# Optimization experiments

Measured on AMD Instinct MI355X. Metric: run time of the kernel, lower is better.

Reference implementation:

```python
import jax, jax.numpy as jnp
import numpy as np

NEG_SLOPE = 0.2
N_NODES = 50000
N_EDGES = 800000
IN_DIM = 256
HID_DIM = 256
HEADS = 8
HEAD_DIM = HID_DIM // HEADS


def setup_inputs() -> dict:
    key = jax.random.key(0)
    ks = jax.random.split(key, 12)
    def glorot(k, shape):
        fan = sum(shape[-2:]) if len(shape) > 1 else shape[-1] + 1
        return jax.random.normal(k, shape, jnp.float32) * jnp.sqrt(2.0 / fan)
    return {
        "data": jax.random.normal(ks[0], (N_NODES, IN_DIM), jnp.float32),
        "src": jax.random.randint(ks[1], (N_EDGES,), 0, N_NODES),
        "dst": jax.random.randint(ks[2], (N_EDGES,), 0, N_NODES),
        "W1": glorot(ks[3], (IN_DIM, HID_DIM)),
        "al1": glorot(ks[4], (HEADS, HEAD_DIM)),
        "ar1": glorot(ks[5], (HEADS, HEAD_DIM)),
        "b1": jnp.zeros((HID_DIM,), jnp.float32),
        "W2": glorot(ks[6], (HID_DIM, HID_DIM)),
        "al2": glorot(ks[7], (HEADS, HEAD_DIM)),
        "ar2": glorot(ks[8], (HEADS, HEAD_DIM)),
        "b2": jnp.zeros((HID_DIM,), jnp.float32),
    }


def gat_layer(x, src, dst, W, al, ar, b):
    """One DGL-style GATConv layer with ReLU activation."""
    N = x.shape[0]
    feat = (x @ W).reshape(N, HEADS, HEAD_DIM)            # [N,H,D]
    el = jnp.sum(feat * al[None], axis=-1)                # [N,H]
    er = jnp.sum(feat * ar[None], axis=-1)                # [N,H]
    e = el[src] + er[dst]                                  # [E,H]
    e = jnp.where(e > 0, e, NEG_SLOPE * e)                 # LeakyReLU(0.2)
    # segment softmax over incoming edges of each dst node
    m = jax.ops.segment_max(e, dst, num_segments=N)        # [N,H] (-inf for empty)
    a = jnp.exp(e - m[dst])                                # [E,H]
    denom = jax.ops.segment_sum(a, dst, num_segments=N)    # [N,H]
    alpha = a / denom[dst]                                 # [E,H]
    msg = feat[src] * alpha[:, :, None]                    # [E,H,D]
    out = jax.ops.segment_sum(msg, dst, num_segments=N)    # [N,H,D]
    out = out + b.reshape(1, HEADS, HEAD_DIM)
    out = jax.nn.relu(out)
    return out.reshape(N, HID_DIM)


def reference(data, src, dst, W1, al1, ar1, b1, W2, al2, ar2, b2):
    h = gat_layer(data, src, dst, W1, al1, ar1, b1)
    h = gat_layer(h, src, dst, W2, al2, ar2, b2)
    return h
```

## Files before the change

kernel.cpp:

```cpp
#include <hip/hip_runtime.h>

#define N_NODES 50000
#define N_EDGES 800000
#define DIM 256
#define HEADS 8
#define NEG_SLOPE 0.2f

typedef unsigned short u16;
typedef float floatx4 __attribute__((ext_vector_type(4)));
typedef __bf16 bf16x8 __attribute__((ext_vector_type(8)));

__device__ __forceinline__ float b2f(u16 u) {
    union { unsigned int i; float f; } v; v.i = ((unsigned int)u) << 16; return v.f;
}
__device__ __forceinline__ u16 f2b(float f) {
    union { float f; unsigned int i; } v; v.f = f;
    unsigned int x = v.i;
    if ((x & 0x7f800000u) == 0x7f800000u && (x & 0x007fffffu)) {
        return (u16)((x >> 16) | 0x0040u);
    }
    unsigned int r = (x + 0x7fffu + ((x >> 16) & 1u)) >> 16;
    return (u16)r;
}

__global__ __launch_bounds__(256) void fill_u32(unsigned int* __restrict__ p,
                                                unsigned int v, int n) {
    int i = blockIdx.x * 256 + threadIdx.x;
    if (i < n) p[i] = v;
}

__global__ __launch_bounds__(256) void init_kernel(const unsigned int* __restrict__ d,
                                                   int* __restrict__ counts,
                                                   int* __restrict__ flag) {
    int i = blockIdx.x * 256 + threadIdx.x;
    if (i < N_NODES) counts[i] = 0;
    if (blockIdx.x == 0) {
        __shared__ int cnt;
        if (threadIdx.x == 0) cnt = 0;
        __syncthreads();
        unsigned int w = d[threadIdx.x];
        int bad = 0;
        #pragma unroll
        for (int half = 0; half < 2; ++half) {
            u16 u = (u16)(w >> (16 * half));
            unsigned int e = (u >> 7) & 0xFFu;
            if (u != 0 && (e >= 141u || e <= 27u)) bad = 1;
        }
        atomicAdd(&cnt, bad);
        __syncthreads();
        if (threadIdx.x == 0) *flag = (cnt > 64) ? 1 : 0;
    }
}

__global__ __launch_bounds__(256) void prep_kernel(const void* __restrict__ W1,
                                                   const void* __restrict__ W2,
                                                   const void* __restrict__ data,
                                                   u16* __restrict__ Wt1,
                                                   u16* __restrict__ Wt2,
                                                   u16* __restrict__ datab,
                                                   const int* __restrict__ flagp) {
    const int isf = *flagp;
    int b = blockIdx.x;
    if (b < 32) {
        const void* W = (b < 16) ? W1 : W2;
        u16* Wt = (b < 16) ? Wt1 : Wt2;
        int t = b & 15;
        int k0 = (t >> 2) * 64, n0 = (t & 3) * 64;
        __shared__ float lt[64][65];
        int c = threadIdx.x & 63, r0 = threadIdx.x >> 6;
        #pragma unroll
        for (int j = 0; j < 16; ++j) {
            int r = j * 4 + r0;
            lt[r][c] = isf ? ((const float*)W)[(k0 + r) * 256 + n0 + c]
                           : b2f(((const u16*)W)[(k0 + r) * 256 + n0 + c]);
        }
        __syncthreads();
        #pragma unroll
        for (int j = 0; j < 16; ++j) {
            int rn = j * 4 + r0;
            Wt[(n0 + rn) * 256 + k0 + c] = f2b(lt[c][rn]);
        }
    } else {
        if (!isf) return;
        int base = (b - 32) * 2048 + threadIdx.x * 8;
        const float* df = (const float*)data + base;
        float4 f0 = *(const float4*)df;
        float4 f1 = *(const float4*)(df + 4);
        u16 tb[8] = {f2b(f0.x), f2b(f0.y), f2b(f0.z), f2b(f0.w),
                     f2b(f1.x), f2b(f1.y), f2b(f1.z), f2b(f1.w)};
        *(uint4*)(datab + base) = *(uint4*)tb;
    }
}

__global__ __launch_bounds__(256) void hist_kernel(const int* __restrict__ dst,
                                                   int* __restrict__ counts, int E) {
    int i = blockIdx.x * 256 + threadIdx.x;
    if (i < E) atomicAdd(&counts[dst[i]], 1);
}

__global__ __launch_bounds__(256) void scan_partial(const int* __restrict__ counts,
                                                    int* __restrict__ partial, int n) {
    int b = blockIdx.x, tid = threadIdx.x;
    int base = b * 1024 + tid * 4;
    int s = 0;
    #pragma unroll
    for (int k = 0; k < 4; ++k) if (base + k < n) s += counts[base + k];
    int lane = tid & 63;
    #pragma unroll
    for (int off = 32; off; off >>= 1) s += __shfl_xor(s, off);
    __shared__ int wsum[4];
    if (lane == 0) wsum[tid >> 6] = s;
    __syncthreads();
    if (tid == 0) partial[b] = wsum[0] + wsum[1] + wsum[2] + wsum[3];
}

__global__ __launch_bounds__(64) void scan_offsets(const int* __restrict__ partial,
                                                   int* __restrict__ offsets,
                                                   int* __restrict__ row_ptr,
                                                   int nb, int n) {
    int t = threadIdx.x;
    int v0 = (t < nb) ? partial[t] : 0;
    int v = v0;
    #pragma unroll
    for (int d = 1; d < 64; d <<= 1) {
        int u = __shfl_up(v, d);
        if (t >= d) v += u;
    }
    if (t < nb) offsets[t] = v - v0;
    if (t == 63) row_ptr[n] = v;
}

__global__ __launch_bounds__(256) void scan_write(const int* __restrict__ counts,
                                                  const int* __restrict__ offsets,
                                                  int* __restrict__ row_ptr,
                                                  int* __restrict__ wptr, int n) {
    int b = blockIdx.x, tid = threadIdx.x;
    int base = b * 1024 + tid * 4;
    int v[4]; int s = 0;
    #pragma unroll
    for (int k = 0; k < 4; ++k) { v[k] = (base + k < n) ? counts[base + k] : 0; s += v[k]; }
    int lane = tid & 63, w = tid >> 6;
    int incl = s;
    #pragma unroll
    for (int d = 1; d < 64; d <<= 1) {
        int u = __shfl_up(incl, d);
        if (lane >= d) incl += u;
    }
    __shared__ int wsum[4];
    if (lane == 63) wsum[w] = incl;
    __syncthreads();
    int woff = 0;
    for (int i = 0; i < w; ++i) woff += wsum[i];
    int run = offsets[b] + woff + incl - s;
    #pragma unroll
    for (int k = 0; k < 4; ++k) {
        if (base + k < n) { row_ptr[base + k] = run; wptr[base + k] = run; run += v[k]; }
    }
}

__global__ __launch_bounds__(256) void scatter_kernel(const int* __restrict__ src,
                                                      const int* __restrict__ dst,
                                                      int* __restrict__ wptr,
                                                      int* __restrict__ src_sorted, int E) {
    int i = blockIdx.x * 256 + threadIdx.x;
    if (i < E) {
        int pos = atomicAdd(&wptr[dst[i]], 1);
        src_sorted[pos] = src[i];
    }
}

#define LDA 264
#define LDB 40

__global__ __launch_bounds__(256, 2) void gemm_fused(const u16* __restrict__ Aisf,
                                                     const u16* __restrict__ Abf,
                                                     const u16* __restrict__ Wt,
                                                     u16* __restrict__ outF,
                                                     float* __restrict__ el,
                                                     float* __restrict__ er,
                                                     const void* __restrict__ al,
                                                     const void* __restrict__ ar,
                                                     int M, const int* __restrict__ flagp) {
    const int isf = *flagp;
    const u16* A = isf ? Aisf : Abf;
    __shared__ u16 As[64][LDA];
    __shared__ u16 Ws[256][LDB];
    const int tid  = threadIdx.x;
    const int w    = tid >> 6;
    const int lane = tid & 63;
    const int quad = lane >> 4;
    const int l16  = lane & 15;
    const int m0   = blockIdx.x * 64;

    #pragma unroll
    for (int it = 0; it < 8; ++it) {
        int idx = it * 256 + tid;
        int r = idx >> 5;
        int c = (idx & 31) << 3;
        int gr = m0 + r;
        if (gr < M) {
            *(uint4*)&As[r][c] = *(const uint4*)(A + gr * 256 + c);
        } else {
            uint4 z = {0u, 0u, 0u, 0u};
            *(uint4*)&As[r][c] = z;
        }
    }

    floatx4 acc[4][4] = {};

    for (int s = 0; s < 8; ++s) {
        __syncthreads();
        #pragma unroll
        for (int it = 0; it < 4; ++it) {
            int idx = it * 256 + tid;
            int n = idx >> 2;
            int k8 = (idx & 3) << 3;
            *(uint4*)&Ws[n][k8] = *(const uint4*)(Wt + n * 256 + s * 32 + k8);
        }
        __syncthreads();

        bf16x8 af[4], bfv[4];
        #pragma unroll
        for (int i = 0; i < 4; ++i)
            af[i] = *(const bf16x8*)&As[16 * i + l16][s * 32 + quad * 8];
        #pragma unroll
        for (int t = 0; t < 4; ++t)
            bfv[t] = *(const bf16x8*)&Ws[64 * w + 16 * t + l16][quad * 8];
        #pragma unroll
        for (int i = 0; i < 4; ++i)
            #pragma unroll
            for (int t = 0; t < 4; ++t)
                acc[i][t] = __builtin_amdgcn_mfma_f32_16x16x32_bf16(af[i], bfv[t], acc[i][t], 0, 0, 0);
    }

    #pragma unroll
    for (int i = 0; i < 4; ++i)
        #pragma unroll
        for (int t = 0; t < 4; ++t)
            #pragma unroll
            for (int r = 0; r < 4; ++r) {
                int row = m0 + 16 * i + quad * 4 + r;
                if (row < M) outF[row * 256 + 64 * w + 16 * t + l16] = f2b(acc[i][t][r]);
            }

    float alv[4], arv[4];
    #pragma unroll
    for (int t = 0; t < 4; ++t) {
        int c = 64 * w + 16 * t + l16;
        alv[t] = isf ? ((const float*)al)[c] : b2f(((const u16*)al)[c]);
        arv[t] = isf ? ((const float*)ar)[c] : b2f(((const u16*)ar)[c]);
    }
    #pragma unroll
    for (int i = 0; i < 4; ++i)
        #pragma unroll
        for (int r = 0; r < 4; ++r) {
            int row = m0 + 16 * i + quad * 4 + r;
            #pragma unroll
            for (int tt = 0; tt < 2; ++tt) {
                float pl = acc[i][2 * tt][r] * alv[2 * tt] + acc[i][2 * tt + 1][r] * alv[2 * tt + 1];
                float pr = acc[i][2 * tt][r] * arv[2 * tt] + acc[i][2 * tt + 1][r] * arv[2 * tt + 1];
                #pragma unroll
                for (int mask = 1; mask <= 8; mask <<= 1) {
                    pl += __shfl_xor(pl, mask);
                    pr += __shfl_xor(pr, mask);
                }
                if (l16 == 0 && row < M) {
                    el[row * 8 + 2 * w + tt] = pl;
                    er[row * 8 + 2 * w + tt] = pr;
                }
            }
        }
}

__global__ __launch_bounds__(256) void aggregate_kernel(const u16* __restrict__ feat,
                                                        const float* __restrict__ el,
                                                        const float* __restrict__ er,
                                                        const void* __restrict__ bias,
                                                        const int* __restrict__ row_ptr,
                                                        const int* __restrict__ src_sorted,
                                                        void* __restrict__ out,
                                                        int out_mode,
                                                        const int* __restrict__ flagp) {
    const int isf = *flagp;
    const int lane = threadIdx.x & 63;
    const int node = blockIdx.x * 4 + (threadIdx.x >> 6);
    if (node >= N_NODES) return;
    const int h = lane >> 3;
    const int j = lane & 7;
    const int beg = row_ptr[node];
    const int deg = row_ptr[node + 1] - beg;
    const float ern = er[node * HEADS + h];

    float m = -1e30f, ssum = 0.f;
    for (int i = j; i < deg; i += 8) {
        int s = src_sorted[beg + i];
        float e = el[s * 8 + h] + ern;
        e = e > 0.f ? e : NEG_SLOPE * e;
        float mn = fmaxf(m, e);
        ssum = ssum * __expf(m - mn) + __expf(e - mn);
        m = mn;
    }
    #pragma unroll
    for (int mask = 1; mask <= 4; mask <<= 1) {
        float mo = __shfl_xor(m, mask);
        float so = __shfl_xor(ssum, mask);
        float mn = fmaxf(m, mo);
        ssum = ssum * __expf(m - mn) + so * __expf(mo - mn);
        m = mn;
    }
    const float mx = m;
    const float inv = ssum > 0.f ? 1.f / ssum : 0.f;

    const int q = lane & 31;
    const int half = lane >> 5;
    const int hq = q >> 2;
    float a[8] = {};
    for (int c0 = 0; c0 < deg; c0 += 8) {
        int i = c0 + j;
        int s = 0; float av = 0.f;
        if (i < deg) {
            s = src_sorted[beg + i];
            float e = el[s * 8 + h] + ern;
            e = e > 0.f ? e : NEG_SLOPE * e;
            av = __expf(e - mx) * inv;
        }
        int rem = deg - c0; if (rem > 8) rem = 8;
        for (int t2 = 0; t2 < rem; t2 += 2) {
            int sel = hq * 8 + t2 + half;
            int   se = __shfl(s, sel);
            float ae = __shfl(av, sel);
            uint4 f = *(const uint4*)(feat + se * DIM + 8 * q);
            a[0] += ae * b2f((u16)(f.x & 0xffffu)); a[1] += ae * b2f((u16)(f.x >> 16));
            a[2] += ae * b2f((u16)(f.y & 0xffffu)); a[3] += ae * b2f((u16)(f.y >> 16));
            a[4] += ae * b2f((u16)(f.z & 0xffffu)); a[5] += ae * b2f((u16)(f.z >> 16));
            a[6] += ae * b2f((u16)(f.w & 0xffffu)); a[7] += ae * b2f((u16)(f.w >> 16));
        }
    }
    #pragma unroll
    for (int k = 0; k < 8; ++k) a[k] += __shfl_xor(a[k], 32);

    if (half == 0) {
        float o[8];
        if (isf) {
            float4 b0 = *(const float4*)((const float*)bias + 8 * q);
            float4 b1 = *(const float4*)((const float*)bias + 8 * q + 4);
            o[0] = a[0] + b0.x; o[1] = a[1] + b0.y; o[2] = a[2] + b0.z; o[3] = a[3] + b0.w;
            o[4] = a[4] + b1.x; o[5] = a[5] + b1.y; o[6] = a[6] + b1.z; o[7] = a[7] + b1.w;
        } else {
            uint4 bu = *(const uint4*)((const u16*)bias + 8 * q);
            o[0] = a[0] + b2f((u16)(bu.x & 0xffffu)); o[1] = a[1] + b2f((u16)(bu.x >> 16));
            o[2] = a[2] + b2f((u16)(bu.y & 0xffffu)); o[3] = a[3] + b2f((u16)(bu.y >> 16));
            o[4] = a[4] + b2f((u16)(bu.z & 0xffffu)); o[5] = a[5] + b2f((u16)(bu.z >> 16));
            o[6] = a[6] + b2f((u16)(bu.w & 0xffffu)); o[7] = a[7] + b2f((u16)(bu.w >> 16));
        }
        #pragma unroll
        for (int k = 0; k < 8; ++k) o[k] = fmaxf(o[k], 0.f);
        if (out_mode == 0 || !isf) {
            u16 pk[8] = {f2b(o[0]), f2b(o[1]), f2b(o[2]), f2b(o[3]),
                         f2b(o[4]), f2b(o[5]), f2b(o[6]), f2b(o[7])};
            *(uint4*)((u16*)out + node * DIM + 8 * q) = *(uint4*)pk;
        } else {
            float4 v0 = {o[0], o[1], o[2], o[3]};
            float4 v1 = {o[4], o[5], o[6], o[7]};
            *(float4*)((float*)out + node * DIM + 8 * q) = v0;
            *(float4*)((float*)out + node * DIM + 8 * q + 4) = v1;
        }
    }
}

extern "C" void kernel_launch(void* const* d_in, const int* in_sizes, int n_in,
                              void* d_out, int out_size, void* d_ws, size_t ws_size,
                              hipStream_t stream) {
    const void* data = d_in[0];
    const int* src = (const int*)d_in[1];
    const int* dst = (const int*)d_in[2];
    const void* W1  = d_in[3];
    const void* al1 = d_in[4];
    const void* ar1 = d_in[5];
    const void* b1  = d_in[6];
    const void* W2  = d_in[7];
    const void* al2 = d_in[8];
    const void* ar2 = d_in[9];
    const void* b2  = d_in[10];

    const size_t NEEDED =
        (size_t)N_NODES * DIM * 2 +
        (size_t)N_NODES * HEADS * 4 * 2 +
        (size_t)N_NODES * 4 * 2 +
        (size_t)(N_NODES + 4) * 4 +
        (size_t)N_EDGES * 4 +
        2 * 256 * 256 * 2 +
        1024;

    if (ws_size < NEEDED) {
        int nwords = (out_size + 1) / 2;
        fill_u32<<<(nwords + 255) / 256, 256, 0, stream>>>(
            (unsigned int*)d_out, 0x42C842C8u, nwords);
        return;
    }

    char* ws = (char*)d_ws;
    u16* feat = (u16*)ws;        ws += (size_t)N_NODES * DIM * 2;
    float* el = (float*)ws;      ws += (size_t)N_NODES * HEADS * 4;
    float* er = (float*)ws;      ws += (size_t)N_NODES * HEADS * 4;
    int* counts = (int*)ws;      ws += (size_t)N_NODES * 4;
    int* wptr = (int*)ws;        ws += (size_t)N_NODES * 4;
    int* row_ptr = (int*)ws;     ws += (size_t)(N_NODES + 4) * 4;
    int* src_sorted = (int*)ws;  ws += (size_t)N_EDGES * 4;
    u16* Wt1 = (u16*)ws;         ws += 256 * 256 * 2;
    u16* Wt2 = (u16*)ws;         ws += 256 * 256 * 2;
    int* partial = (int*)ws;     ws += 256;
    int* offsets = (int*)ws;     ws += 256;
    int* flag = (int*)ws;        ws += 256;

    u16* h1    = (u16*)d_out;
    u16* datab = (u16*)d_out + (size_t)N_NODES * DIM;

    const int nb = (N_NODES + 1023) / 1024;

    init_kernel<<<(N_NODES + 255) / 256, 256, 0, stream>>>(
        (const unsigned int*)data, counts, flag);
    prep_kernel<<<32 + (N_NODES * DIM) / 2048, 256, 0, stream>>>(
        W1, W2, data, Wt1, Wt2, datab, flag);
    hist_kernel<<<(N_EDGES + 255) / 256, 256, 0, stream>>>(dst, counts, N_EDGES);
    scan_partial<<<nb, 256, 0, stream>>>(counts, partial, N_NODES);
    scan_offsets<<<1, 64, 0, stream>>>(partial, offsets, row_ptr, nb, N_NODES);
    scan_write<<<nb, 256, 0, stream>>>(counts, offsets, row_ptr, wptr, N_NODES);
    scatter_kernel<<<(N_EDGES + 255) / 256, 256, 0, stream>>>(src, dst, wptr, src_sorted, N_EDGES);

    const int gemm_blocks = (N_NODES + 63) / 64;
    const int agg_blocks = (N_NODES + 3) / 4;

    gemm_fused<<<gemm_blocks, 256, 0, stream>>>(datab, (const u16*)data, Wt1, feat,
                                                el, er, al1, ar1, N_NODES, flag);
    aggregate_kernel<<<agg_blocks, 256, 0, stream>>>(feat, el, er, b1, row_ptr, src_sorted,
                                                     (void*)h1, 0, flag);
    gemm_fused<<<gemm_blocks, 256, 0, stream>>>(h1, h1, Wt2, feat,
                                                el, er, al2, ar2, N_NODES, flag);
    aggregate_kernel<<<agg_blocks, 256, 0, stream>>>(feat, el, er, b2, row_ptr, src_sorted,
                                                     d_out, 2, flag);
}
```

Baseline: 437.2 us.

## Split aggregation across head-quarters and cache edge scores in shared memory

The aggregation kernel now launches four times as many blocks, and each wave handles one node for only two heads (a quarter of the feature columns), with 32 lanes per head in the softmax reduction. Source indices and edge logits for the first 96 edges are cached in LDS and turned into normalised attention weights once, so the weighted-sum loop reads them instead of recomputing from el. Each feature gather becomes a 16-byte slice per lane covering 8 edges at a time. The cost is four times the src_sorted/el reads per node across blocks, plus extra cross-lane reductions.

```diff
diff --git a/kernel.cpp b/kernel.cpp
--- a/kernel.cpp
+++ b/kernel.cpp
@@ -5,6 +5,7 @@
 #define DIM 256
 #define HEADS 8
 #define NEG_SLOPE 0.2f
+#define CAP 96
 
 typedef unsigned short u16;
 typedef float floatx4 __attribute__((ext_vector_type(4)));
@@ -282,72 +283,116 @@
                                                         int out_mode,
                                                         const int* __restrict__ flagp) {
     const int isf = *flagp;
+    const int NB4 = (N_NODES + 3) / 4;
+    const int qtr = blockIdx.x / NB4;
+    const int wv = threadIdx.x >> 6;
+    const int node = (blockIdx.x % NB4) * 4 + wv;
+    if (node >= N_NODES) return;
     const int lane = threadIdx.x & 63;
-    const int node = blockIdx.x * 4 + (threadIdx.x >> 6);
-    if (node >= N_NODES) return;
-    const int h = lane >> 3;
-    const int j = lane & 7;
+
+    __shared__ int   sS[4][CAP];
+    __shared__ float sE[4][CAP][2];
+
     const int beg = row_ptr[node];
     const int deg = row_ptr[node + 1] - beg;
-    const float ern = er[node * HEADS + h];
-
+
+    const int half = lane >> 5;
+    const int t = lane & 31;
+    const int h = 2 * qtr + half;
+    const float ern = er[node * 8 + h];
     float m = -1e30f, ssum = 0.f;
-    for (int i = j; i < deg; i += 8) {
+    for (int i = t; i < deg; i += 32) {
         int s = src_sorted[beg + i];
         float e = el[s * 8 + h] + ern;
         e = e > 0.f ? e : NEG_SLOPE * e;
+        if (i < CAP) {
+            if (half == 0) sS[wv][i] = s;
+            sE[wv][i][half] = e;
+        }
         float mn = fmaxf(m, e);
         ssum = ssum * __expf(m - mn) + __expf(e - mn);
         m = mn;
     }
     #pragma unroll
-    for (int mask = 1; mask <= 4; mask <<= 1) {
+    for (int mask = 1; mask <= 16; mask <<= 1) {
         float mo = __shfl_xor(m, mask);
         float so = __shfl_xor(ssum, mask);
         float mn = fmaxf(m, mo);
         ssum = ssum * __expf(m - mn) + so * __expf(mo - mn);
         m = mn;
     }
-    const float mx = m;
     const float inv = ssum > 0.f ? 1.f / ssum : 0.f;
 
-    const int q = lane & 31;
-    const int half = lane >> 5;
-    const int hq = q >> 2;
+    const int dcap = deg < CAP ? deg : CAP;
+    for (int i = t; i < dcap; i += 32) {
+        sE[wv][i][half] = __expf(sE[wv][i][half] - m) * inv;
+    }
+
+    const float mxA = __shfl(m, 0),  invA = __shfl(inv, 0),  ernA = __shfl(ern, 0);
+    const float mxB = __shfl(m, 32), invB = __shfl(inv, 32), ernB = __shfl(ern, 32);
+
+    const int j = lane & 7;
+    const int slot = lane >> 3;
+    const int hsel = j >> 2;
+    const float mxs  = hsel ? mxB : mxA;
+    const float invs = hsel ? invB : invA;
+    const float erns = hsel ? ernB : ernA;
+    const int hidx = 2 * qtr + hsel;
+    const u16* fbase = feat + qtr * 64 + j * 8;
+
     float a[8] = {};
-    for (int c0 = 0; c0 < deg; c0 += 8) {
-        int i = c0 + j;
-        int s = 0; float av = 0.f;
-        if (i < deg) {
-            s = src_sorted[beg + i];
-            float e = el[s * 8 + h] + ern;
-            e = e > 0.f ? e : NEG_SLOPE * e;
-            av = __expf(e - mx) * inv;
-        }
-        int rem = deg - c0; if (rem > 8) rem = 8;
-        for (int t2 = 0; t2 < rem; t2 += 2) {
-            int sel = hq * 8 + t2 + half;
-            int   se = __shfl(s, sel);
-            float ae = __shfl(av, sel);
-            uint4 f = *(const uint4*)(feat + se * DIM + 8 * q);
-            a[0] += ae * b2f((u16)(f.x & 0xffffu)); a[1] += ae * b2f((u16)(f.x >> 16));
-            a[2] += ae * b2f((u16)(f.y & 0xffffu)); a[3] += ae * b2f((u16)(f.y >> 16));
-            a[4] += ae * b2f((u16)(f.z & 0xffffu)); a[5] += ae * b2f((u16)(f.z >> 16));
-            a[6] += ae * b2f((u16)(f.w & 0xffffu)); a[7] += ae * b2f((u16)(f.w >> 16));
-        }
-    }
-    #pragma unroll
-    for (int k = 0; k < 8; ++k) a[k] += __shfl_xor(a[k], 32);
-
-    if (half == 0) {
+    for (int c0 = 0; c0 < deg; c0 += 16) {
+        int iA = c0 + slot;
+        int iB = c0 + 8 + slot;
+        int sA = 0, sB = 0;
+        float aeA = 0.f, aeB = 0.f;
+        if (iA < deg) {
+            if (iA < CAP) { sA = sS[wv][iA]; aeA = sE[wv][iA][hsel]; }
+            else {
+                sA = src_sorted[beg + iA];
+                float e = el[sA * 8 + hidx] + erns;
+                e = e > 0.f ? e : NEG_SLOPE * e;
+                aeA = __expf(e - mxs) * invs;
+            }
+        }
+        if (iB < deg) {
+            if (iB < CAP) { sB = sS[wv][iB]; aeB = sE[wv][iB][hsel]; }
+            else {
+                sB = src_sorted[beg + iB];
+                float e = el[sB * 8 + hidx] + erns;
+                e = e > 0.f ? e : NEG_SLOPE * e;
+                aeB = __expf(e - mxs) * invs;
+            }
+        }
+        uint4 fA = *(const uint4*)(fbase + (size_t)sA * DIM);
+        uint4 fB = *(const uint4*)(fbase + (size_t)sB * DIM);
+        a[0] += aeA * b2f((u16)(fA.x & 0xffffu)); a[1] += aeA * b2f((u16)(fA.x >> 16));
+        a[2] += aeA * b2f((u16)(fA.y & 0xffffu)); a[3] += aeA * b2f((u16)(fA.y >> 16));
+        a[4] += aeA * b2f((u16)(fA.z & 0xffffu)); a[5] += aeA * b2f((u16)(fA.z >> 16));
+        a[6] += aeA * b2f((u16)(fA.w & 0xffffu)); a[7] += aeA * b2f((u16)(fA.w >> 16));
+        a[0] += aeB * b2f((u16)(fB.x & 0xffffu)); a[1] += aeB * b2f((u16)(fB.x >> 16));
+        a[2] += aeB * b2f((u16)(fB.y & 0xffffu)); a[3] += aeB * b2f((u16)(fB.y >> 16));
+        a[4] += aeB * b2f((u16)(fB.z & 0xffffu)); a[5] += aeB * b2f((u16)(fB.z >> 16));
+        a[6] += aeB * b2f((u16)(fB.w & 0xffffu)); a[7] += aeB * b2f((u16)(fB.w >> 16));
+    }
+
+    #pragma unroll
+    for (int k = 0; k < 8; ++k) {
+        a[k] += __shfl_xor(a[k], 8);
+        a[k] += __shfl_xor(a[k], 16);
+        a[k] += __shfl_xor(a[k], 32);
+    }
+
+    if (slot == 0) {
+        const int c = qtr * 64 + j * 8;
         float o[8];
         if (isf) {
-            float4 b0 = *(const float4*)((const float*)bias + 8 * q);
-            float4 b1 = *(const float4*)((const float*)bias + 8 * q + 4);
+            float4 b0 = *(const float4*)((const float*)bias + c);
+            float4 b1 = *(const float4*)((const float*)bias + c + 4);
             o[0] = a[0] + b0.x; o[1] = a[1] + b0.y; o[2] = a[2] + b0.z; o[3] = a[3] + b0.w;
             o[4] = a[4] + b1.x; o[5] = a[5] + b1.y; o[6] = a[6] + b1.z; o[7] = a[7] + b1.w;
         } else {
-            uint4 bu = *(const uint4*)((const u16*)bias + 8 * q);
+            uint4 bu = *(const uint4*)((const u16*)bias + c);
             o[0] = a[0] + b2f((u16)(bu.x & 0xffffu)); o[1] = a[1] + b2f((u16)(bu.x >> 16));
             o[2] = a[2] + b2f((u16)(bu.y & 0xffffu)); o[3] = a[3] + b2f((u16)(bu.y >> 16));
             o[4] = a[4] + b2f((u16)(bu.z & 0xffffu)); o[5] = a[5] + b2f((u16)(bu.z >> 16));
@@ -358,12 +403,12 @@
         if (out_mode == 0 || !isf) {
             u16 pk[8] = {f2b(o[0]), f2b(o[1]), f2b(o[2]), f2b(o[3]),
                          f2b(o[4]), f2b(o[5]), f2b(o[6]), f2b(o[7])};
-            *(uint4*)((u16*)out + node * DIM + 8 * q) = *(uint4*)pk;
+            *(uint4*)((u16*)out + (size_t)node * DIM + c) = *(uint4*)pk;
         } else {
             float4 v0 = {o[0], o[1], o[2], o[3]};
             float4 v1 = {o[4], o[5], o[6], o[7]};
-            *(float4*)((float*)out + node * DIM + 8 * q) = v0;
-            *(float4*)((float*)out + node * DIM + 8 * q + 4) = v1;
+            *(float4*)((float*)out + (size_t)node * DIM + c) = v0;
+            *(float4*)((float*)out + (size_t)node * DIM + c + 4) = v1;
         }
     }
 }
@@ -429,7 +474,7 @@
     scatter_kernel<<<(N_EDGES + 255) / 256, 256, 0, stream>>>(src, dst, wptr, src_sorted, N_EDGES);
 
     const int gemm_blocks = (N_NODES + 63) / 64;
-    const int agg_blocks = (N_NODES + 3) / 4;
+    const int agg_blocks = 4 * ((N_NODES + 3) / 4);
 
     gemm_fused<<<gemm_blocks, 256, 0, stream>>>(datab, (const u16*)data, Wt1, feat,
                                                 el, er, al1, ar1, N_NODES, flag);
```

After: 503.3 us. 15.1% more time.

## Software-pipeline feature gathers and split softmax stats into two chains

Applied to the files above, without the earlier changes.

The max/sum pass now keeps two independent online-softmax accumulators, processing two edges per iteration to expose more memory-level parallelism for the el gathers. The aggregation loop prefetches the next chunk of 8 edges' indices, weights and feature rows (4 loads per lane) while the current chunk is accumulated, and handles partial chunks by padding with zero-weight reads of row 0. This is meant to hide gather latency, at the cost of more registers and redundant loads of node 0's features for padded slots. Output addressing is widened to size_t.

```diff
diff --git a/kernel.cpp b/kernel.cpp
--- a/kernel.cpp
+++ b/kernel.cpp
@@ -291,15 +291,26 @@
     const int deg = row_ptr[node + 1] - beg;
     const float ern = er[node * HEADS + h];
 
-    float m = -1e30f, ssum = 0.f;
-    for (int i = j; i < deg; i += 8) {
-        int s = src_sorted[beg + i];
-        float e = el[s * 8 + h] + ern;
-        e = e > 0.f ? e : NEG_SLOPE * e;
-        float mn = fmaxf(m, e);
-        ssum = ssum * __expf(m - mn) + __expf(e - mn);
-        m = mn;
-    }
+    float m0v = -1e30f, ss0 = 0.f;
+    float m1v = -1e30f, ss1 = 0.f;
+    for (int i = j; i < deg; i += 16) {
+        int s0 = src_sorted[beg + i];
+        int i2 = i + 8;
+        int s1 = (i2 < deg) ? src_sorted[beg + i2] : 0;
+        float e0 = el[s0 * 8 + h] + ern;
+        float e1 = el[s1 * 8 + h] + ern;
+        e0 = e0 > 0.f ? e0 : NEG_SLOPE * e0;
+        e1 = e1 > 0.f ? e1 : NEG_SLOPE * e1;
+        if (i2 >= deg) e1 = -3e30f;
+        float mn0 = fmaxf(m0v, e0);
+        ss0 = ss0 * __expf(m0v - mn0) + __expf(e0 - mn0);
+        m0v = mn0;
+        float mn1 = fmaxf(m1v, e1);
+        ss1 = ss1 * __expf(m1v - mn1) + __expf(e1 - mn1);
+        m1v = mn1;
+    }
+    float m = fmaxf(m0v, m1v);
+    float ssum = ss0 * __expf(m0v - m) + ss1 * __expf(m1v - m);
     #pragma unroll
     for (int mask = 1; mask <= 4; mask <<= 1) {
         float mo = __shfl_xor(m, mask);
@@ -315,27 +326,55 @@
     const int half = lane >> 5;
     const int hq = q >> 2;
     float a[8] = {};
+
+    int sC = 0; float avC = 0.f;
+    if (j < deg) {
+        sC = src_sorted[beg + j];
+        float e = el[sC * 8 + h] + ern;
+        e = e > 0.f ? e : NEG_SLOPE * e;
+        avC = __expf(e - mx) * inv;
+    }
+    uint4 f[4]; float ae[4];
+    #pragma unroll
+    for (int u = 0; u < 4; ++u) {
+        int sel = hq * 8 + 2 * u + half;
+        int se = __shfl(sC, sel);
+        ae[u] = __shfl(avC, sel);
+        f[u] = *(const uint4*)(feat + (size_t)se * DIM + 8 * q);
+    }
+
+    #pragma unroll 2
     for (int c0 = 0; c0 < deg; c0 += 8) {
-        int i = c0 + j;
-        int s = 0; float av = 0.f;
-        if (i < deg) {
-            s = src_sorted[beg + i];
-            float e = el[s * 8 + h] + ern;
-            e = e > 0.f ? e : NEG_SLOPE * e;
-            av = __expf(e - mx) * inv;
-        }
-        int rem = deg - c0; if (rem > 8) rem = 8;
-        for (int t2 = 0; t2 < rem; t2 += 2) {
-            int sel = hq * 8 + t2 + half;
-            int   se = __shfl(s, sel);
-            float ae = __shfl(av, sel);
-            uint4 f = *(const uint4*)(feat + se * DIM + 8 * q);
-            a[0] += ae * b2f((u16)(f.x & 0xffffu)); a[1] += ae * b2f((u16)(f.x >> 16));
-            a[2] += ae * b2f((u16)(f.y & 0xffffu)); a[3] += ae * b2f((u16)(f.y >> 16));
-            a[4] += ae * b2f((u16)(f.z & 0xffffu)); a[5] += ae * b2f((u16)(f.z >> 16));
-            a[6] += ae * b2f((u16)(f.w & 0xffffu)); a[7] += ae * b2f((u16)(f.w >> 16));
-        }
-    }
+        uint4 f2[4]; float ae2[4];
+        {
+            int sN = 0; float avN = 0.f;
+            int i = c0 + 8 + j;
+            if (i < deg) {
+                sN = src_sorted[beg + i];
+                float e = el[sN * 8 + h] + ern;
+                e = e > 0.f ? e : NEG_SLOPE * e;
+                avN = __expf(e - mx) * inv;
+            }
+            #pragma unroll
+            for (int u = 0; u < 4; ++u) {
+                int sel = hq * 8 + 2 * u + half;
+                int se = __shfl(sN, sel);
+                ae2[u] = __shfl(avN, sel);
+                f2[u] = *(const uint4*)(feat + (size_t)se * DIM + 8 * q);
+            }
+        }
+        #pragma unroll
+        for (int u = 0; u < 4; ++u) {
+            float w = ae[u];
+            a[0] += w * b2f((u16)(f[u].x & 0xffffu)); a[1] += w * b2f((u16)(f[u].x >> 16));
+            a[2] += w * b2f((u16)(f[u].y & 0xffffu)); a[3] += w * b2f((u16)(f[u].y >> 16));
+            a[4] += w * b2f((u16)(f[u].z & 0xffffu)); a[5] += w * b2f((u16)(f[u].z >> 16));
+            a[6] += w * b2f((u16)(f[u].w & 0xffffu)); a[7] += w * b2f((u16)(f[u].w >> 16));
+        }
+        #pragma unroll
+        for (int u = 0; u < 4; ++u) { f[u] = f2[u]; ae[u] = ae2[u]; }
+    }
+
     #pragma unroll
     for (int k = 0; k < 8; ++k) a[k] += __shfl_xor(a[k], 32);
 
@@ -358,12 +397,12 @@
         if (out_mode == 0 || !isf) {
             u16 pk[8] = {f2b(o[0]), f2b(o[1]), f2b(o[2]), f2b(o[3]),
                          f2b(o[4]), f2b(o[5]), f2b(o[6]), f2b(o[7])};
-            *(uint4*)((u16*)out + node * DIM + 8 * q) = *(uint4*)pk;
+            *(uint4*)((u16*)out + (size_t)node * DIM + 8 * q) = *(uint4*)pk;
         } else {
             float4 v0 = {o[0], o[1], o[2], o[3]};
             float4 v1 = {o[4], o[5], o[6], o[7]};
-            *(float4*)((float*)out + node * DIM + 8 * q) = v0;
-            *(float4*)((float*)out + node * DIM + 8 * q + 4) = v1;
+            *(float4*)((float*)out + (size_t)node * DIM + 8 * q) = v0;
+            *(float4*)((float*)out + (size_t)node * DIM + 8 * q + 4) = v1;
         }
     }
 }
```

Result: no change. 437.3 us (+0.0%).
